# Optimization experiments

Measured on AMD Instinct MI355X. Metric: run time of the kernel, lower is better.

Reference implementation:

```python
import jax, jax.numpy as jnp
import numpy as np

B, S, D, E, K = 4, 2048, 1024, 8, 2
EPS, W_THRES, TEMP = 1e-4, 0.1, 1.0


def setup_inputs() -> dict:
    key = jax.random.key(0)
    k1, k2, k3, k4, k5 = jax.random.split(key, 5)
    x = jax.random.normal(k1, (B, S, D), dtype=jnp.float32)
    gate_W = jax.random.normal(k2, (D, E), dtype=jnp.float32) * 0.02
    gate_b = jnp.zeros((E,), dtype=jnp.float32)
    expert_W = jax.random.normal(k3, (E, D, D), dtype=jnp.float32) * 0.02
    expert_b = jnp.zeros((E, D), dtype=jnp.float32)
    return {"x": x, "gate_W": gate_W, "gate_b": gate_b,
            "expert_W": expert_W, "expert_b": expert_b}


def reference(x, gate_W, gate_b, expert_W, expert_b):
    # Gating: linear -> temperature -> clamp-min(eps) -> softmax
    scores = jnp.maximum((x @ gate_W + gate_b) / TEMP, EPS)      # [B,S,E]
    p = jax.nn.softmax(scores, axis=-1)                           # [B,S,E]
    _, topk_idx = jax.lax.top_k(p, K)                             # [B,S,K]
    # boolean membership mask of selected experts
    topk_mask = jax.nn.one_hot(topk_idx, E, dtype=p.dtype).sum(-2) > 0  # [B,S,E]
    # weights: clamp-min(weight_thres), normalized by detached sum over selected
    w = jnp.maximum(p, W_THRES)                                   # [B,S,E]
    w_gather = jnp.take_along_axis(w, topk_idx, axis=-1)          # [B,S,K]
    total = jax.lax.stop_gradient(w_gather.sum(-1, keepdims=True))
    w = w / total
    comb = jnp.where(topk_mask, w, jnp.zeros_like(w))             # [B,S,E]
    # Dense equivalent of gather/expert/scatter loop (E small): each expert
    # is Linear(D, D); masked combine weights zero out unselected experts.
    y = jnp.einsum('bsd,edf->bsef', x, expert_W) + expert_b       # [B,S,E,D]
    out = jnp.einsum('bsef,bse->bsf', y, comb) / K                # [B,S,D]
    return out
```

## Files before the change

kernel.cpp:

```cpp
#include <hip/hip_runtime.h>
#include <hip/hip_fp16.h>
#include <stdint.h>

#define TOK 8192
#define DIM 1024
#define NE 8
#define NTILE 136
#define NCT 4

typedef short bf16x8 __attribute__((ext_vector_type(8)));
typedef float f32x4 __attribute__((ext_vector_type(4)));

__device__ __forceinline__ unsigned short f2bf(float f) {
  unsigned int u = __float_as_uint(f);
  u += 0x7FFFu + ((u >> 16) & 1u);
  return (unsigned short)(u >> 16);
}

__device__ __forceinline__ void gl_lds16(const void* g, void* l) {
  __builtin_amdgcn_global_load_lds(
      (__attribute__((address_space(1))) unsigned int*)(g),
      (__attribute__((address_space(3))) unsigned int*)(l), 16, 0, 0);
}

__global__ __launch_bounds__(256) void gate_kernel(
    const float* __restrict__ x, const float* __restrict__ gW,
    const float* __restrict__ gb, unsigned short* __restrict__ xb,
    int* __restrict__ eSel, float* __restrict__ wSel, int* __restrict__ cnt)
{
  if (blockIdx.x == 0 && threadIdx.x < NE) cnt[threadIdx.x] = 0;

  __shared__ float gWs[NE * DIM];
#pragma unroll
  for (int h = 0; h < 8; ++h) {
    const int m = threadIdx.x + h * 256;
    float4 v = ((const float4*)gW)[m];
    const int d = m >> 1, e0 = (m & 1) * 4;
    gWs[(e0 + 0) * DIM + d] = v.x;
    gWs[(e0 + 1) * DIM + d] = v.y;
    gWs[(e0 + 2) * DIM + d] = v.z;
    gWs[(e0 + 3) * DIM + d] = v.w;
  }
  __syncthreads();

  const int wave = threadIdx.x >> 6;
  const int lane = threadIdx.x & 63;
  const int t = blockIdx.x * 4 + wave;
  const float4* xrow = (const float4*)(x + (size_t)t * DIM);
  ushort4* xbrow = (ushort4*)(xb + (size_t)t * DIM);

  double acc[NE];
#pragma unroll
  for (int e = 0; e < NE; ++e) acc[e] = 0.0;

#pragma unroll
  for (int i = 0; i < 4; ++i) {
    const int j = i * 64 + lane;
    float4 v = xrow[j];
    ushort4 pk;
    pk.x = f2bf(v.x); pk.y = f2bf(v.y); pk.z = f2bf(v.z); pk.w = f2bf(v.w);
    xbrow[j] = pk;
#pragma unroll
    for (int e = 0; e < NE; ++e) {
      float4 gv = *(const float4*)&gWs[e * DIM + j * 4];
      acc[e] += (double)v.x * (double)gv.x + (double)v.y * (double)gv.y
              + (double)v.z * (double)gv.z + (double)v.w * (double)gv.w;
    }
  }
#pragma unroll
  for (int off = 32; off > 0; off >>= 1) {
#pragma unroll
    for (int e = 0; e < NE; ++e)
      acc[e] += __shfl_xor(acc[e], off, 64);
  }

  if (lane == 0) {
    double s[NE];
#pragma unroll
    for (int e = 0; e < NE; ++e) {
      s[e] = acc[e] + (double)gb[e];
      if (s[e] < 1e-4) s[e] = 1e-4;
    }
    int e0 = 0;
    for (int e = 1; e < NE; ++e) if (s[e] > s[e0]) e0 = e;
    int e1 = (e0 == 0) ? 1 : 0;
    for (int e = 0; e < NE; ++e) if (e != e0 && s[e] > s[e1]) e1 = e;
    float m = (float)s[e0];
    float Z = 0.f, pf[NE];
#pragma unroll
    for (int e = 0; e < NE; ++e) { pf[e] = __expf((float)s[e] - m); Z += pf[e]; }
    float w0 = pf[e0] / Z; if (w0 < 0.1f) w0 = 0.1f;
    float w1 = pf[e1] / Z; if (w1 < 0.1f) w1 = 0.1f;
    const float inv = 0.5f / (w0 + w1);
    eSel[t * 2 + 0] = e0;
    eSel[t * 2 + 1] = e1;
    wSel[t * 2 + 0] = w0 * inv;
    wSel[t * 2 + 1] = w1 * inv;
  }
}

__global__ __launch_bounds__(256) void scatter_kernel(
    const int* __restrict__ eSel, const float* __restrict__ wSel,
    int* __restrict__ cnt, int* __restrict__ listTok, float* __restrict__ listW)
{
  __shared__ int lcnt[NE];
  __shared__ int base[NE];
  const int tid = threadIdx.x;
  if (tid < NE) lcnt[tid] = 0;
  __syncthreads();

  const int t = blockIdx.x * 256 + tid;
  const int e0 = eSel[t * 2 + 0];
  const int e1 = eSel[t * 2 + 1];
  const float w0 = wSel[t * 2 + 0];
  const float w1 = wSel[t * 2 + 1];
  const int l0 = atomicAdd(&lcnt[e0], 1);
  const int l1 = atomicAdd(&lcnt[e1], 1);
  __syncthreads();
  if (tid < NE) base[tid] = atomicAdd(&cnt[tid], lcnt[tid]);
  __syncthreads();

  const int p0 = base[e0] + l0;
  listTok[e0 * TOK + p0] = t * 2 + 0;
  listW [e0 * TOK + p0] = w0;
  const int p1 = base[e1] + l1;
  listTok[e1 * TOK + p1] = t * 2 + 1;
  listW [e1 * TOK + p1] = w1;
}

__global__ __launch_bounds__(256) void transpose_w(
    const float* __restrict__ W, unsigned short* __restrict__ Wt)
{
  __shared__ float t2[64][65];
  const int b  = blockIdx.x;
  const int e  = b >> 8;
  const int db = (b >> 4) & 15;
  const int fb = b & 15;
  const int d0 = db * 64, f0 = fb * 64;
  const int tid = threadIdx.x;
#pragma unroll
  for (int h = 0; h < 4; ++h) {
    const int idx = tid + h * 256;
    const int r = idx >> 4, c4 = idx & 15;
    float4 v = *(const float4*)&W[((size_t)e * DIM + d0 + r) * DIM + f0 + c4 * 4];
    t2[r][c4 * 4 + 0] = v.x;
    t2[r][c4 * 4 + 1] = v.y;
    t2[r][c4 * 4 + 2] = v.z;
    t2[r][c4 * 4 + 3] = v.w;
  }
  __syncthreads();
#pragma unroll
  for (int h = 0; h < 8; ++h) {
    const int o = tid + h * 256;
    const int f = o >> 5, k2 = (o & 31) * 2;
    const unsigned int lo = f2bf(t2[k2][f]);
    const unsigned int hi = f2bf(t2[k2 + 1][f]);
    *(unsigned int*)&Wt[((size_t)e * DIM + f0 + f) * DIM + d0 + k2] =
        lo | (hi << 16);
  }
}

#define WAITVM(n) asm volatile("s_waitcnt vmcnt(" #n ")" ::: "memory")

#define STG3(t, h, stb)                                                      \
  { const int off_ = (t) * 64 + (h) * 32;                                    \
    unsigned short* Ad_ = (unsigned short*)As + ((stb) * 2 + (h)) * (128 * 32) + w * 512;  \
    unsigned short* Bd_ = (unsigned short*)Bs + ((stb) * 2 + (h)) * (256 * 32) + w * 1024; \
    gl_lds16(srcA  + off_, Ad_);                                             \
    gl_lds16(srcB0 + off_, Bd_);                                             \
    gl_lds16(srcB1 + off_, Bd_ + 512); }

#define PHASE(t, h, bufv, stb, DO_STAGE, VMA)                                \
  { const unsigned short* Ab_ = (const unsigned short*)As + ((bufv) * 2 + (h)) * (128 * 32); \
    const unsigned short* Bb_ = (const unsigned short*)Bs + ((bufv) * 2 + (h)) * (256 * 32); \
    bf16x8 af[4], bfr[4];                                                    \
    _Pragma("unroll")                                                        \
    for (int mt = 0; mt < 4; ++mt)                                           \
      af[mt] = *(const bf16x8*)&Ab_[(wr * 64 + mt * 16 + mrow) * 32 + sA];   \
    _Pragma("unroll")                                                        \
    for (int nt = 0; nt < 4; ++nt)                                           \
      bfr[nt] = *(const bf16x8*)&Bb_[(wc * 64 + nt * 16 + mrow) * 32 + sA];  \
    if (DO_STAGE) { STG3((t) + 2, h, stb); }                                 \
    __builtin_amdgcn_s_barrier();                                            \
    __builtin_amdgcn_s_setprio(1);                                           \
    _Pragma("unroll")                                                        \
    for (int mt = 0; mt < 4; ++mt)                                           \
      _Pragma("unroll")                                                      \
      for (int nt = 0; nt < 4; ++nt)                                         \
        acc[mt][nt] = __builtin_amdgcn_mfma_f32_16x16x32_bf16(               \
            af[mt], bfr[nt], acc[mt][nt], 0, 0, 0);                          \
    __builtin_amdgcn_s_setprio(0);                                           \
    VMA;                                                                     \
    __builtin_amdgcn_s_barrier(); }

__global__ __launch_bounds__(512, 2) void moe_gemm(
    const unsigned short* __restrict__ xb, const unsigned short* __restrict__ Wt,
    const float* __restrict__ eb, const int* __restrict__ cnt,
    const int* __restrict__ listTok, const float* __restrict__ listW,
    __half* __restrict__ yslot)
{
  const int dId = blockIdx.x % NTILE;
  const int cT  = blockIdx.x / NTILE;
  int e = -1, r0 = 0, rows = 0, accT = 0;
#pragma unroll
  for (int ee = 0; ee < NE; ++ee) {
    const int c = cnt[ee];
    const int nt = (c + 127) >> 7;
    if (dId >= accT && dId < accT + nt) {
      e = ee; r0 = (dId - accT) * 128;
      rows = c - r0; if (rows > 128) rows = 128;
    }
    accT += nt;
  }
  if (e < 0) return;

  __shared__ __align__(16) unsigned short As[3 * 2 * 128 * 32];
  __shared__ __align__(16) unsigned short Bs[3 * 2 * 256 * 32];
  __shared__ int   tid_s[128];
  __shared__ float w_s[128];

  const int tid = threadIdx.x;
  if (tid < 128) {
    if (tid < rows) {
      tid_s[tid] = listTok[e * TOK + r0 + tid];
      w_s[tid]   = listW [e * TOK + r0 + tid];
    } else {
      tid_s[tid] = 0;
      w_s[tid]   = 0.0f;
    }
  }
  __syncthreads();

  const int w    = tid >> 6;
  const int lane = tid & 63;
  const int rA  = w * 16 + (lane >> 2);
  const int qA  = (lane & 3) ^ (rA & 3);
  const unsigned short* srcA = xb + (size_t)(tid_s[rA] >> 1) * DIM + qA * 8;
  const int rB0 = w * 32 + (lane >> 2);
  const int rB1 = rB0 + 16;
  const int qB  = (lane & 3) ^ (rB0 & 3);
  const unsigned short* srcB0 = Wt + ((size_t)e * DIM + cT * 256 + rB0) * DIM + qB * 8;
  const unsigned short* srcB1 = Wt + ((size_t)e * DIM + cT * 256 + rB1) * DIM + qB * 8;

  const int wr = w >> 2, wc = w & 3;
  const int mrow = lane & 15;
  const int qg   = lane >> 4;
  const int sA   = (qg ^ (mrow & 3)) * 8;

  f32x4 acc[4][4];
#pragma unroll
  for (int i = 0; i < 4; ++i)
#pragma unroll
    for (int j = 0; j < 4; ++j)
      acc[i][j] = {0.f, 0.f, 0.f, 0.f};

  STG3(0, 0, 0); STG3(0, 1, 0); STG3(1, 0, 1); STG3(1, 1, 1);
  WAITVM(9);
  __builtin_amdgcn_s_barrier();

  int buf = 0, stb = 2;
#pragma unroll 1
  for (int t = 0; t < 14; ++t) {
    PHASE(t, 0, buf, stb, true, WAITVM(9));
    PHASE(t, 1, buf, stb, true, WAITVM(9));
    buf = (buf == 2) ? 0 : buf + 1;
    stb = (stb == 2) ? 0 : stb + 1;
  }
  PHASE(14, 0, 2, 0, false, WAITVM(6));
  PHASE(14, 1, 2, 0, false, WAITVM(3));
  PHASE(15, 0, 0, 0, false, WAITVM(0));
  PHASE(15, 1, 0, 0, false, ((void)0));

  const int colBase = cT * 256 + wc * 64 + mrow;
  float bias[4];
#pragma unroll
  for (int nt = 0; nt < 4; ++nt)
    bias[nt] = eb[(size_t)e * DIM + colBase + nt * 16];
#pragma unroll
  for (int mt = 0; mt < 4; ++mt) {
#pragma unroll
    for (int r = 0; r < 4; ++r) {
      const int rloc = wr * 64 + mt * 16 + (lane >> 4) * 4 + r;
      if (rloc < rows) {
        const int tk    = tid_s[rloc];
        const float wgt = w_s[rloc];
        __half* dst = yslot + ((size_t)(tk & 1) * TOK + (size_t)(tk >> 1)) * DIM;
#pragma unroll
        for (int nt = 0; nt < 4; ++nt)
          dst[colBase + nt * 16] = __float2half(wgt * (acc[mt][nt][r] + bias[nt]));
      }
    }
  }
}

__global__ __launch_bounds__(256) void combine(
    const __half* __restrict__ y0, const __half* __restrict__ y1,
    float4* __restrict__ out)
{
  const size_t i = (size_t)blockIdx.x * 256 + threadIdx.x;
  const ushort4 ua = ((const ushort4*)y0)[i];
  const ushort4 ub = ((const ushort4*)y1)[i];
  const __half* ah = (const __half*)&ua;
  const __half* bh = (const __half*)&ub;
  float4 o;
  o.x = __half2float(ah[0]) + __half2float(bh[0]);
  o.y = __half2float(ah[1]) + __half2float(bh[1]);
  o.z = __half2float(ah[2]) + __half2float(bh[2]);
  o.w = __half2float(ah[3]) + __half2float(bh[3]);
  out[i] = o;
}

extern "C" void kernel_launch(void* const* d_in, const int* in_sizes, int n_in,
                              void* d_out, int out_size, void* d_ws, size_t ws_size,
                              hipStream_t stream)
{
  const float* x  = (const float*)d_in[0];
  const float* gW = (const float*)d_in[1];
  const float* gb = (const float*)d_in[2];
  const float* eW = (const float*)d_in[3];
  const float* eb = (const float*)d_in[4];
  float* out = (float*)d_out;

  char* p = (char*)d_ws;
  unsigned short* xb = (unsigned short*)p;  p += (size_t)TOK * DIM * 2;
  unsigned short* Wt = (unsigned short*)p;  p += (size_t)NE * DIM * DIM * 2;
  __half* yslot = (__half*)p;               p += (size_t)2 * TOK * DIM * 2;
  int* cnt = (int*)p;                       p += 256;
  int* listTok = (int*)p;                   p += (size_t)NE * TOK * 4;
  float* listW = (float*)p;                 p += (size_t)NE * TOK * 4;

  int*   eSel = (int*)yslot;
  float* wSel = (float*)((char*)yslot + TOK * 8);

  gate_kernel<<<TOK / 4, 256, 0, stream>>>(x, gW, gb, xb, eSel, wSel, cnt);
  scatter_kernel<<<TOK / 256, 256, 0, stream>>>(eSel, wSel, cnt, listTok, listW);
  transpose_w<<<NE * 256, 256, 0, stream>>>(eW, Wt);
  moe_gemm<<<NTILE * NCT, 512, 0, stream>>>(xb, Wt, eb, cnt, listTok, listW, yslot);
  combine<<<TOK * DIM / 4 / 256, 256, 0, stream>>>(
      yslot, yslot + (size_t)TOK * DIM, (float4*)out);
}
```

Before: 208.3 us.

## Retile MoE GEMM to 256x128 tiles with 4 waves and single-barrier pipeline

```diff
diff --git a/kernel.cpp b/kernel.cpp
--- a/kernel.cpp
+++ b/kernel.cpp
@@ -5,8 +5,8 @@
 #define TOK 8192
 #define DIM 1024
 #define NE 8
-#define NTILE 136
-#define NCT 4
+#define NT 72
+#define NCT 8
 
 typedef short bf16x8 __attribute__((ext_vector_type(8)));
 typedef float f32x4 __attribute__((ext_vector_type(4)));
@@ -162,125 +162,125 @@
 
 #define WAITVM(n) asm volatile("s_waitcnt vmcnt(" #n ")" ::: "memory")
 
-#define STG3(t, h, stb)                                                      \
-  { const int off_ = (t) * 64 + (h) * 32;                                    \
-    unsigned short* Ad_ = (unsigned short*)As + ((stb) * 2 + (h)) * (128 * 32) + w * 512;  \
-    unsigned short* Bd_ = (unsigned short*)Bs + ((stb) * 2 + (h)) * (256 * 32) + w * 1024; \
-    gl_lds16(srcA  + off_, Ad_);                                             \
-    gl_lds16(srcB0 + off_, Bd_);                                             \
-    gl_lds16(srcB1 + off_, Bd_ + 512); }
-
-#define PHASE(t, h, bufv, stb, DO_STAGE, VMA)                                \
-  { const unsigned short* Ab_ = (const unsigned short*)As + ((bufv) * 2 + (h)) * (128 * 32); \
-    const unsigned short* Bb_ = (const unsigned short*)Bs + ((bufv) * 2 + (h)) * (256 * 32); \
-    bf16x8 af[4], bfr[4];                                                    \
+#define STG(kt, bs)                                                          \
+  { const int off_ = (kt) * 32;                                              \
+    gl_lds16(srcA0 + off_, &As[bs][w * 2048 + 0]);                           \
+    gl_lds16(srcA1 + off_, &As[bs][w * 2048 + 512]);                         \
+    gl_lds16(srcA2 + off_, &As[bs][w * 2048 + 1024]);                        \
+    gl_lds16(srcA3 + off_, &As[bs][w * 2048 + 1536]);                        \
+    gl_lds16(srcB0 + off_, &Bs[bs][w * 1024 + 0]);                           \
+    gl_lds16(srcB1 + off_, &Bs[bs][w * 1024 + 512]); }
+
+#define CMP(bs)                                                              \
+  { const unsigned short* Ab_ = &As[bs][0];                                  \
+    const unsigned short* Bb_ = &Bs[bs][0];                                  \
+    bf16x8 af[8], bfr[4];                                                    \
     _Pragma("unroll")                                                        \
-    for (int mt = 0; mt < 4; ++mt)                                           \
-      af[mt] = *(const bf16x8*)&Ab_[(wr * 64 + mt * 16 + mrow) * 32 + sA];   \
+    for (int mt = 0; mt < 8; ++mt)                                           \
+      af[mt] = *(const bf16x8*)&Ab_[rdA + mt * 512];                         \
     _Pragma("unroll")                                                        \
     for (int nt = 0; nt < 4; ++nt)                                           \
-      bfr[nt] = *(const bf16x8*)&Bb_[(wc * 64 + nt * 16 + mrow) * 32 + sA];  \
-    if (DO_STAGE) { STG3((t) + 2, h, stb); }                                 \
-    __builtin_amdgcn_s_barrier();                                            \
+      bfr[nt] = *(const bf16x8*)&Bb_[rdB + nt * 512];                        \
     __builtin_amdgcn_s_setprio(1);                                           \
     _Pragma("unroll")                                                        \
-    for (int mt = 0; mt < 4; ++mt)                                           \
+    for (int mt = 0; mt < 8; ++mt)                                           \
       _Pragma("unroll")                                                      \
       for (int nt = 0; nt < 4; ++nt)                                         \
         acc[mt][nt] = __builtin_amdgcn_mfma_f32_16x16x32_bf16(               \
             af[mt], bfr[nt], acc[mt][nt], 0, 0, 0);                          \
-    __builtin_amdgcn_s_setprio(0);                                           \
-    VMA;                                                                     \
-    __builtin_amdgcn_s_barrier(); }
-
-__global__ __launch_bounds__(512, 2) void moe_gemm(
+    __builtin_amdgcn_s_setprio(0); }
+
+__global__ __launch_bounds__(256, 2) void moe_gemm(
     const unsigned short* __restrict__ xb, const unsigned short* __restrict__ Wt,
     const float* __restrict__ eb, const int* __restrict__ cnt,
     const int* __restrict__ listTok, const float* __restrict__ listW,
     __half* __restrict__ yslot)
 {
-  const int dId = blockIdx.x % NTILE;
-  const int cT  = blockIdx.x / NTILE;
+  const int dId = blockIdx.x % NT;
+  const int cT  = blockIdx.x / NT;
   int e = -1, r0 = 0, rows = 0, accT = 0;
 #pragma unroll
   for (int ee = 0; ee < NE; ++ee) {
     const int c = cnt[ee];
-    const int nt = (c + 127) >> 7;
+    const int nt = (c + 255) >> 8;
     if (dId >= accT && dId < accT + nt) {
-      e = ee; r0 = (dId - accT) * 128;
-      rows = c - r0; if (rows > 128) rows = 128;
+      e = ee; r0 = (dId - accT) * 256;
+      rows = c - r0; if (rows > 256) rows = 256;
     }
     accT += nt;
   }
   if (e < 0) return;
 
-  __shared__ __align__(16) unsigned short As[3 * 2 * 128 * 32];
-  __shared__ __align__(16) unsigned short Bs[3 * 2 * 256 * 32];
-  __shared__ int   tid_s[128];
-  __shared__ float w_s[128];
+  __shared__ __align__(16) unsigned short As[3][256 * 32];
+  __shared__ __align__(16) unsigned short Bs[3][128 * 32];
+  __shared__ int   tid_s[256];
+  __shared__ float w_s[256];
 
   const int tid = threadIdx.x;
-  if (tid < 128) {
-    if (tid < rows) {
-      tid_s[tid] = listTok[e * TOK + r0 + tid];
-      w_s[tid]   = listW [e * TOK + r0 + tid];
-    } else {
-      tid_s[tid] = 0;
-      w_s[tid]   = 0.0f;
-    }
+  if (tid < rows) {
+    tid_s[tid] = listTok[e * TOK + r0 + tid];
+    w_s[tid]   = listW [e * TOK + r0 + tid];
+  } else {
+    tid_s[tid] = 0;
+    w_s[tid]   = 0.0f;
   }
   __syncthreads();
 
   const int w    = tid >> 6;
   const int lane = tid & 63;
-  const int rA  = w * 16 + (lane >> 2);
-  const int qA  = (lane & 3) ^ (rA & 3);
-  const unsigned short* srcA = xb + (size_t)(tid_s[rA] >> 1) * DIM + qA * 8;
-  const int rB0 = w * 32 + (lane >> 2);
-  const int rB1 = rB0 + 16;
-  const int qB  = (lane & 3) ^ (rB0 & 3);
-  const unsigned short* srcB0 = Wt + ((size_t)e * DIM + cT * 256 + rB0) * DIM + qB * 8;
-  const unsigned short* srcB1 = Wt + ((size_t)e * DIM + cT * 256 + rB1) * DIM + qB * 8;
-
-  const int wr = w >> 2, wc = w & 3;
+  const int qsrc = (lane & 3) ^ ((lane >> 3) & 3);
+  const int lr   = lane >> 2;
+  const unsigned short* srcA0 = xb + (size_t)(tid_s[w * 64 +  0 + lr] >> 1) * DIM + qsrc * 8;
+  const unsigned short* srcA1 = xb + (size_t)(tid_s[w * 64 + 16 + lr] >> 1) * DIM + qsrc * 8;
+  const unsigned short* srcA2 = xb + (size_t)(tid_s[w * 64 + 32 + lr] >> 1) * DIM + qsrc * 8;
+  const unsigned short* srcA3 = xb + (size_t)(tid_s[w * 64 + 48 + lr] >> 1) * DIM + qsrc * 8;
+  const unsigned short* srcB0 = Wt + ((size_t)e * DIM + cT * 128 + w * 32 +  0 + lr) * DIM + qsrc * 8;
+  const unsigned short* srcB1 = Wt + ((size_t)e * DIM + cT * 128 + w * 32 + 16 + lr) * DIM + qsrc * 8;
+
+  const int wr = w >> 1, wc = w & 1;
   const int mrow = lane & 15;
   const int qg   = lane >> 4;
-  const int sA   = (qg ^ (mrow & 3)) * 8;
-
-  f32x4 acc[4][4];
-#pragma unroll
-  for (int i = 0; i < 4; ++i)
+  const int s8   = (qg ^ ((mrow >> 1) & 3)) * 8;
+  const int rdA  = (wr * 128 + mrow) * 32 + s8;
+  const int rdB  = (wc * 64 + mrow) * 32 + s8;
+
+  f32x4 acc[8][4];
+#pragma unroll
+  for (int i = 0; i < 8; ++i)
 #pragma unroll
     for (int j = 0; j < 4; ++j)
       acc[i][j] = {0.f, 0.f, 0.f, 0.f};
 
-  STG3(0, 0, 0); STG3(0, 1, 0); STG3(1, 0, 1); STG3(1, 1, 1);
-  WAITVM(9);
+  STG(0, 0);
+  STG(1, 1);
+  WAITVM(6);
   __builtin_amdgcn_s_barrier();
 
-  int buf = 0, stb = 2;
+  int bC = 0, bS = 2;
 #pragma unroll 1
-  for (int t = 0; t < 14; ++t) {
-    PHASE(t, 0, buf, stb, true, WAITVM(9));
-    PHASE(t, 1, buf, stb, true, WAITVM(9));
-    buf = (buf == 2) ? 0 : buf + 1;
-    stb = (stb == 2) ? 0 : stb + 1;
-  }
-  PHASE(14, 0, 2, 0, false, WAITVM(6));
-  PHASE(14, 1, 2, 0, false, WAITVM(3));
-  PHASE(15, 0, 0, 0, false, WAITVM(0));
-  PHASE(15, 1, 0, 0, false, ((void)0));
-
-  const int colBase = cT * 256 + wc * 64 + mrow;
+  for (int kt = 0; kt < 30; ++kt) {
+    STG(kt + 2, bS);
+    CMP(bC);
+    WAITVM(6);
+    __builtin_amdgcn_s_barrier();
+    bC = (bC == 2) ? 0 : bC + 1;
+    bS = (bS == 2) ? 0 : bS + 1;
+  }
+  CMP(0);
+  WAITVM(0);
+  __builtin_amdgcn_s_barrier();
+  CMP(1);
+
+  const int colBase = cT * 128 + wc * 64 + mrow;
   float bias[4];
 #pragma unroll
   for (int nt = 0; nt < 4; ++nt)
     bias[nt] = eb[(size_t)e * DIM + colBase + nt * 16];
 #pragma unroll
-  for (int mt = 0; mt < 4; ++mt) {
+  for (int mt = 0; mt < 8; ++mt) {
 #pragma unroll
     for (int r = 0; r < 4; ++r) {
-      const int rloc = wr * 64 + mt * 16 + (lane >> 4) * 4 + r;
+      const int rloc = wr * 128 + mt * 16 + (lane >> 4) * 4 + r;
       if (rloc < rows) {
         const int tk    = tid_s[rloc];
         const float wgt = w_s[rloc];
@@ -335,7 +335,7 @@
   gate_kernel<<<TOK / 4, 256, 0, stream>>>(x, gW, gb, xb, eSel, wSel, cnt);
   scatter_kernel<<<TOK / 256, 256, 0, stream>>>(eSel, wSel, cnt, listTok, listW);
   transpose_w<<<NE * 256, 256, 0, stream>>>(eW, Wt);
-  moe_gemm<<<NTILE * NCT, 512, 0, stream>>>(xb, Wt, eb, cnt, listTok, listW, yslot);
+  moe_gemm<<<NT * NCT, 256, 0, stream>>>(xb, Wt, eb, cnt, listTok, listW, yslot);
   combine<<<TOK * DIM / 4 / 256, 256, 0, stream>>>(
       yslot, yslot + (size_t)TOK * DIM, (float4*)out);
 }
```

Result: no change. 208.0 us (-0.1%).
